# Performance work log

Measured on AMD Instinct MI355X. Metric: run time of the kernel, lower is better.

## Reference

```python
import jax, jax.numpy as jnp
import numpy as np

B, D, H, W, C = 2, 160, 160, 160, 3


def _grid(d, h, w, dtype=jnp.float32):
    # identity coordinate grid, shape [d, h, w, 3]
    gx, gy, gz = jnp.meshgrid(jnp.arange(d, dtype=dtype),
                              jnp.arange(h, dtype=dtype),
                              jnp.arange(w, dtype=dtype), indexing='ij')
    return jnp.stack([gx, gy, gz], axis=-1)


def _trilinear(vol, loc):
    """Trilinear sample vol [D,H,W,C] at float coords loc [D,H,W,3] (border-clipped)."""
    d, h, w, c = vol.shape
    sizes = jnp.array([d, h, w], dtype=loc.dtype)
    loc = jnp.clip(loc, 0.0, sizes - 1.0)
    loc0 = jnp.floor(loc)
    wgt = loc - loc0                                   # fractional part, [D,H,W,3]
    i0 = loc0.astype(jnp.int32)
    i1 = jnp.minimum(i0 + 1, jnp.array([d - 1, h - 1, w - 1], dtype=jnp.int32))
    vol_flat = vol.reshape(-1, c)                      # [D*H*W, C]

    def flat(ix, iy, iz):
        return (ix * h + iy) * w + iz

    out = jnp.zeros(loc.shape[:-1] + (c,), dtype=vol.dtype)
    for bx in (0, 1):
        ix = i0[..., 0] if bx == 0 else i1[..., 0]
        wx = (1.0 - wgt[..., 0]) if bx == 0 else wgt[..., 0]
        for by in (0, 1):
            iy = i0[..., 1] if by == 0 else i1[..., 1]
            wy = (1.0 - wgt[..., 1]) if by == 0 else wgt[..., 1]
            for bz in (0, 1):
                iz = i0[..., 2] if bz == 0 else i1[..., 2]
                wz = (1.0 - wgt[..., 2]) if bz == 0 else wgt[..., 2]
                corner = jnp.take(vol_flat, flat(ix, iy, iz), axis=0)
                out = out + corner * (wx * wy * wz)[..., None]
    return out


def setup_inputs() -> dict:
    key = jax.random.key(0)
    k1, k2 = jax.random.split(key)
    warp1 = jax.random.normal(k1, (B, D, H, W, C), dtype=jnp.float32)
    warp2 = jax.random.normal(k2, (B, D, H, W, C), dtype=jnp.float32)
    return {"warp1": warp1, "warp2": warp2}


def reference(warp1, warp2):
    # Compose dense transforms applied in order [warp1, warp2]:
    #   u(x) = u2(x) + u1(x + u2(x))   (trilinear resample of u1)
    grid = _grid(D, H, W, dtype=warp1.dtype)

    def compose_pair(u1, u2):
        return u2 + _trilinear(u1, grid + u2)

    return jax.vmap(compose_pair)(warp1, warp2)
```

## Files before the change

kernel.cpp:

```cpp
#include <hip/hip_runtime.h>

constexpr int Bn = 2;
constexpr int Dn = 160;
constexpr int Hn = 160;
constexpr int Wn = 160;
constexpr int NV = Bn * Dn * Hn * Wn;
constexpr int VOL = Dn * Hn * Wn;

__global__ __launch_bounds__(256) void compose_transform_kernel(
    const float* __restrict__ warp1,
    const float* __restrict__ warp2,
    float* __restrict__ out) {
    int idx = blockIdx.x * blockDim.x + threadIdx.x;
    if (idx >= NV) return;

    int w  = idx % Wn;
    int t  = idx / Wn;
    int h  = t % Hn;
    t      = t / Hn;
    int d  = t % Dn;
    int b  = t / Dn;

    int base3 = idx * 3;
    float u2x = __builtin_nontemporal_load(warp2 + base3 + 0);
    float u2y = __builtin_nontemporal_load(warp2 + base3 + 1);
    float u2z = __builtin_nontemporal_load(warp2 + base3 + 2);

    float lx = fminf(fmaxf((float)d + u2x, 0.0f), (float)(Dn - 1));
    float ly = fminf(fmaxf((float)h + u2y, 0.0f), (float)(Hn - 1));
    float lz = fminf(fmaxf((float)w + u2z, 0.0f), (float)(Wn - 1));

    int ixb = min((int)floorf(lx), Dn - 2);
    int iyb = min((int)floorf(ly), Hn - 2);
    int izb = min((int)floorf(lz), Wn - 2);

    float wx1 = lx - (float)ixb, wx0 = 1.0f - wx1;
    float wy1 = ly - (float)iyb, wy0 = 1.0f - wy1;
    float wz1 = lz - (float)izb, wz0 = 1.0f - wz1;

    const float* __restrict__ u1 = warp1 + b * (VOL * 3);

    const float* p00 = u1 + ((ixb       * Hn + iyb    ) * Wn + izb) * 3;
    const float* p01 = u1 + ((ixb       * Hn + iyb + 1) * Wn + izb) * 3;
    const float* p10 = u1 + (((ixb + 1) * Hn + iyb    ) * Wn + izb) * 3;
    const float* p11 = u1 + (((ixb + 1) * Hn + iyb + 1) * Wn + izb) * 3;

    float a00_0 = p00[0], a00_1 = p00[1], a00_2 = p00[2];
    float a00_3 = p00[3], a00_4 = p00[4], a00_5 = p00[5];
    float a01_0 = p01[0], a01_1 = p01[1], a01_2 = p01[2];
    float a01_3 = p01[3], a01_4 = p01[4], a01_5 = p01[5];
    float a10_0 = p10[0], a10_1 = p10[1], a10_2 = p10[2];
    float a10_3 = p10[3], a10_4 = p10[4], a10_5 = p10[5];
    float a11_0 = p11[0], a11_1 = p11[1], a11_2 = p11[2];
    float a11_3 = p11[3], a11_4 = p11[4], a11_5 = p11[5];

    float w00 = wx0 * wy0;
    float w01 = wx0 * wy1;
    float w10 = wx1 * wy0;
    float w11 = wx1 * wy1;

    float rx, ry, rz;
    float accx, accy, accz;

    rx = fmaf(wz1, a00_3, wz0 * a00_0);
    ry = fmaf(wz1, a00_4, wz0 * a00_1);
    rz = fmaf(wz1, a00_5, wz0 * a00_2);
    accx = w00 * rx; accy = w00 * ry; accz = w00 * rz;

    rx = fmaf(wz1, a01_3, wz0 * a01_0);
    ry = fmaf(wz1, a01_4, wz0 * a01_1);
    rz = fmaf(wz1, a01_5, wz0 * a01_2);
    accx = fmaf(w01, rx, accx); accy = fmaf(w01, ry, accy); accz = fmaf(w01, rz, accz);

    rx = fmaf(wz1, a10_3, wz0 * a10_0);
    ry = fmaf(wz1, a10_4, wz0 * a10_1);
    rz = fmaf(wz1, a10_5, wz0 * a10_2);
    accx = fmaf(w10, rx, accx); accy = fmaf(w10, ry, accy); accz = fmaf(w10, rz, accz);

    rx = fmaf(wz1, a11_3, wz0 * a11_0);
    ry = fmaf(wz1, a11_4, wz0 * a11_1);
    rz = fmaf(wz1, a11_5, wz0 * a11_2);
    accx = fmaf(w11, rx, accx); accy = fmaf(w11, ry, accy); accz = fmaf(w11, rz, accz);

    __builtin_nontemporal_store(u2x + accx, out + base3 + 0);
    __builtin_nontemporal_store(u2y + accy, out + base3 + 1);
    __builtin_nontemporal_store(u2z + accz, out + base3 + 2);
}

extern "C" void kernel_launch(void* const* d_in, const int* in_sizes, int n_in,
                              void* d_out, int out_size, void* d_ws, size_t ws_size,
                              hipStream_t stream) {
    const float* warp1 = (const float*)d_in[0];
    const float* warp2 = (const float*)d_in[1];
    float* out = (float*)d_out;

    int threads = 256;
    int blocks = (NV + threads - 1) / threads;
    compose_transform_kernel<<<blocks, threads, 0, stream>>>(warp1, warp2, out);
}
```

Baseline: 346.5 us.

## Process four voxels per thread with vectorized I/O and XCD-aware block swizzle

Each thread now handles four consecutive voxels along W. It loads the three float4 words of warp2 and stores the output as three float4 writes instead of scalar accesses. Block indices are remapped so that consecutive chunks of the volume land on the same XCD, which should improve L2 reuse of warp1 gathers. The trade-offs are higher register pressure and fewer blocks in flight, and the code assumes NV divides evenly into blocks of 1024 voxels.

Measured after the change: 426.4 us. +23.1%, slower.

```diff
diff --git a/kernel.cpp b/kernel.cpp
--- a/kernel.cpp
+++ b/kernel.cpp
@@ -4,87 +4,120 @@
 constexpr int Dn = 160;
 constexpr int Hn = 160;
 constexpr int Wn = 160;
-constexpr int NV = Bn * Dn * Hn * Wn;
+constexpr int NV  = Bn * Dn * Hn * Wn;
 constexpr int VOL = Dn * Hn * Wn;
 
-__global__ __launch_bounds__(256) void compose_transform_kernel(
+constexpr int VPT  = 4;
+constexpr int TPB  = 256;
+constexpr int VPB  = VPT * TPB;
+constexpr int NBLK = NV / VPB;
+constexpr int NXCD = 8;
+constexpr int CHUNK = NBLK / NXCD;
+
+typedef float f32x4 __attribute__((ext_vector_type(4)));
+
+__global__ __launch_bounds__(TPB) void compose_transform_kernel(
     const float* __restrict__ warp1,
     const float* __restrict__ warp2,
     float* __restrict__ out) {
-    int idx = blockIdx.x * blockDim.x + threadIdx.x;
-    if (idx >= NV) return;
 
-    int w  = idx % Wn;
-    int t  = idx / Wn;
+    int bid = blockIdx.x;
+    int swz = (bid & (NXCD - 1)) * CHUNK + (bid >> 3);
+
+    int v0 = swz * VPB + (int)threadIdx.x * VPT;
+
+    int w0 = v0 % Wn;
+    int t  = v0 / Wn;
     int h  = t % Hn;
     t      = t / Hn;
     int d  = t % Dn;
     int b  = t / Dn;
 
-    int base3 = idx * 3;
-    float u2x = __builtin_nontemporal_load(warp2 + base3 + 0);
-    float u2y = __builtin_nontemporal_load(warp2 + base3 + 1);
-    float u2z = __builtin_nontemporal_load(warp2 + base3 + 2);
+    const f32x4* w2v = reinterpret_cast<const f32x4*>(warp2 + (size_t)v0 * 3);
+    f32x4 q0 = __builtin_nontemporal_load(w2v + 0);
+    f32x4 q1 = __builtin_nontemporal_load(w2v + 1);
+    f32x4 q2 = __builtin_nontemporal_load(w2v + 2);
 
-    float lx = fminf(fmaxf((float)d + u2x, 0.0f), (float)(Dn - 1));
-    float ly = fminf(fmaxf((float)h + u2y, 0.0f), (float)(Hn - 1));
-    float lz = fminf(fmaxf((float)w + u2z, 0.0f), (float)(Wn - 1));
-
-    int ixb = min((int)floorf(lx), Dn - 2);
-    int iyb = min((int)floorf(ly), Hn - 2);
-    int izb = min((int)floorf(lz), Wn - 2);
-
-    float wx1 = lx - (float)ixb, wx0 = 1.0f - wx1;
-    float wy1 = ly - (float)iyb, wy0 = 1.0f - wy1;
-    float wz1 = lz - (float)izb, wz0 = 1.0f - wz1;
+    float u2[12] = {q0.x, q0.y, q0.z, q0.w,
+                    q1.x, q1.y, q1.z, q1.w,
+                    q2.x, q2.y, q2.z, q2.w};
 
     const float* __restrict__ u1 = warp1 + b * (VOL * 3);
 
-    const float* p00 = u1 + ((ixb       * Hn + iyb    ) * Wn + izb) * 3;
-    const float* p01 = u1 + ((ixb       * Hn + iyb + 1) * Wn + izb) * 3;
-    const float* p10 = u1 + (((ixb + 1) * Hn + iyb    ) * Wn + izb) * 3;
-    const float* p11 = u1 + (((ixb + 1) * Hn + iyb + 1) * Wn + izb) * 3;
+    float res[12];
 
-    float a00_0 = p00[0], a00_1 = p00[1], a00_2 = p00[2];
-    float a00_3 = p00[3], a00_4 = p00[4], a00_5 = p00[5];
-    float a01_0 = p01[0], a01_1 = p01[1], a01_2 = p01[2];
-    float a01_3 = p01[3], a01_4 = p01[4], a01_5 = p01[5];
-    float a10_0 = p10[0], a10_1 = p10[1], a10_2 = p10[2];
-    float a10_3 = p10[3], a10_4 = p10[4], a10_5 = p10[5];
-    float a11_0 = p11[0], a11_1 = p11[1], a11_2 = p11[2];
-    float a11_3 = p11[3], a11_4 = p11[4], a11_5 = p11[5];
+#pragma unroll
+    for (int j = 0; j < VPT; ++j) {
+        float u2x = u2[3 * j + 0];
+        float u2y = u2[3 * j + 1];
+        float u2z = u2[3 * j + 2];
 
-    float w00 = wx0 * wy0;
-    float w01 = wx0 * wy1;
-    float w10 = wx1 * wy0;
-    float w11 = wx1 * wy1;
+        float lx = fminf(fmaxf((float)d + u2x, 0.0f), (float)(Dn - 1));
+        float ly = fminf(fmaxf((float)h + u2y, 0.0f), (float)(Hn - 1));
+        float lz = fminf(fmaxf((float)(w0 + j) + u2z, 0.0f), (float)(Wn - 1));
 
-    float rx, ry, rz;
-    float accx, accy, accz;
+        int ixb = min((int)floorf(lx), Dn - 2);
+        int iyb = min((int)floorf(ly), Hn - 2);
+        int izb = min((int)floorf(lz), Wn - 2);
 
-    rx = fmaf(wz1, a00_3, wz0 * a00_0);
-    ry = fmaf(wz1, a00_4, wz0 * a00_1);
-    rz = fmaf(wz1, a00_5, wz0 * a00_2);
-    accx = w00 * rx; accy = w00 * ry; accz = w00 * rz;
+        float wx1 = lx - (float)ixb, wx0 = 1.0f - wx1;
+        float wy1 = ly - (float)iyb, wy0 = 1.0f - wy1;
+        float wz1 = lz - (float)izb, wz0 = 1.0f - wz1;
 
-    rx = fmaf(wz1, a01_3, wz0 * a01_0);
-    ry = fmaf(wz1, a01_4, wz0 * a01_1);
-    rz = fmaf(wz1, a01_5, wz0 * a01_2);
-    accx = fmaf(w01, rx, accx); accy = fmaf(w01, ry, accy); accz = fmaf(w01, rz, accz);
+        const float* p00 = u1 + ((ixb * Hn + iyb) * Wn + izb) * 3;
+        const float* p01 = p00 + Wn * 3;
+        const float* p10 = p00 + Hn * Wn * 3;
+        const float* p11 = p10 + Wn * 3;
 
-    rx = fmaf(wz1, a10_3, wz0 * a10_0);
-    ry = fmaf(wz1, a10_4, wz0 * a10_1);
-    rz = fmaf(wz1, a10_5, wz0 * a10_2);
-    accx = fmaf(w10, rx, accx); accy = fmaf(w10, ry, accy); accz = fmaf(w10, rz, accz);
+        float a00_0 = p00[0], a00_1 = p00[1], a00_2 = p00[2];
+        float a00_3 = p00[3], a00_4 = p00[4], a00_5 = p00[5];
+        float a01_0 = p01[0], a01_1 = p01[1], a01_2 = p01[2];
+        float a01_3 = p01[3], a01_4 = p01[4], a01_5 = p01[5];
+        float a10_0 = p10[0], a10_1 = p10[1], a10_2 = p10[2];
+        float a10_3 = p10[3], a10_4 = p10[4], a10_5 = p10[5];
+        float a11_0 = p11[0], a11_1 = p11[1], a11_2 = p11[2];
+        float a11_3 = p11[3], a11_4 = p11[4], a11_5 = p11[5];
 
-    rx = fmaf(wz1, a11_3, wz0 * a11_0);
-    ry = fmaf(wz1, a11_4, wz0 * a11_1);
-    rz = fmaf(wz1, a11_5, wz0 * a11_2);
-    accx = fmaf(w11, rx, accx); accy = fmaf(w11, ry, accy); accz = fmaf(w11, rz, accz);
+        float w00 = wx0 * wy0;
+        float w01 = wx0 * wy1;
+        float w10 = wx1 * wy0;
+        float w11 = wx1 * wy1;
 
-    __builtin_nontemporal_store(u2x + accx, out + base3 + 0);
-    __builtin_nontemporal_store(u2y + accy, out + base3 + 1);
-    __builtin_nontemporal_store(u2z + accz, out + base3 + 2);
+        float rx, ry, rz;
+        float accx, accy, accz;
+
+        rx = fmaf(wz1, a00_3, wz0 * a00_0);
+        ry = fmaf(wz1, a00_4, wz0 * a00_1);
+        rz = fmaf(wz1, a00_5, wz0 * a00_2);
+        accx = w00 * rx; accy = w00 * ry; accz = w00 * rz;
+
+        rx = fmaf(wz1, a01_3, wz0 * a01_0);
+        ry = fmaf(wz1, a01_4, wz0 * a01_1);
+        rz = fmaf(wz1, a01_5, wz0 * a01_2);
+        accx = fmaf(w01, rx, accx); accy = fmaf(w01, ry, accy); accz = fmaf(w01, rz, accz);
+
+        rx = fmaf(wz1, a10_3, wz0 * a10_0);
+        ry = fmaf(wz1, a10_4, wz0 * a10_1);
+        rz = fmaf(wz1, a10_5, wz0 * a10_2);
+        accx = fmaf(w10, rx, accx); accy = fmaf(w10, ry, accy); accz = fmaf(w10, rz, accz);
+
+        rx = fmaf(wz1, a11_3, wz0 * a11_0);
+        ry = fmaf(wz1, a11_4, wz0 * a11_1);
+        rz = fmaf(wz1, a11_5, wz0 * a11_2);
+        accx = fmaf(w11, rx, accx); accy = fmaf(w11, ry, accy); accz = fmaf(w11, rz, accz);
+
+        res[3 * j + 0] = u2x + accx;
+        res[3 * j + 1] = u2y + accy;
+        res[3 * j + 2] = u2z + accz;
+    }
+
+    f32x4 o0 = {res[0], res[1], res[2],  res[3]};
+    f32x4 o1 = {res[4], res[5], res[6],  res[7]};
+    f32x4 o2 = {res[8], res[9], res[10], res[11]};
+    f32x4* ov = reinterpret_cast<f32x4*>(out + (size_t)v0 * 3);
+    __builtin_nontemporal_store(o0, ov + 0);
+    __builtin_nontemporal_store(o1, ov + 1);
+    __builtin_nontemporal_store(o2, ov + 2);
 }
 
 extern "C" void kernel_launch(void* const* d_in, const int* in_sizes, int n_in,
@@ -94,7 +127,5 @@
     const float* warp2 = (const float*)d_in[1];
     float* out = (float*)d_out;
 
-    int threads = 256;
-    int blocks = (NV + threads - 1) / threads;
-    compose_transform_kernel<<<blocks, threads, 0, stream>>>(warp1, warp2, out);
+    compose_transform_kernel<<<NBLK, TPB, 0, stream>>>(warp1, warp2, out);
 }
```
